# Performance work log

Measured on AMD Instinct MI355X. Metric: run time of the kernel, lower is better.

The kernel has to match this reference:

```python
import jax, jax.numpy as jnp
import numpy as np
from jax import lax

DIM = 128
NUM_HEADS = 8
GROUP_SPLIT = (4, 4)
DIM_HEAD = DIM // NUM_HEADS  # 16
SCALOR = DIM_HEAD ** (-0.5)
KSIZE = 5
WS = 4
C_HI = GROUP_SPLIT[0] * DIM_HEAD  # 64
C_LO = GROUP_SPLIT[1] * DIM_HEAD  # 64


def conv1x1(x, w, b):
    # x: [b,c,h,w], w: [o,c], b: [o]
    return jnp.einsum('oc,bchw->bohw', w, x) + b[None, :, None, None]


def dwconv(x, w, b):
    # depthwise conv, w: [C,1,k,k]
    C = x.shape[1]
    pad = KSIZE // 2
    y = lax.conv_general_dilated(x, w, window_strides=(1, 1),
                                 padding=((pad, pad), (pad, pad)),
                                 dimension_numbers=('NCHW', 'OIHW', 'NCHW'),
                                 feature_group_count=C)
    return y + b[None, :, None, None]


def avgpool(x, ws):
    b, c, h, w = x.shape
    return x.reshape(b, c, h // ws, ws, w // ws, ws).mean(axis=(3, 5))


def setup_inputs() -> dict:
    key = jax.random.key(0)
    ks = jax.random.split(key, 16)
    s = 0.02
    inp = {
        'x': jax.random.normal(ks[0], (8, DIM, 96, 96), dtype=jnp.float32),
        'qkv_w': jax.random.normal(ks[1], (3 * C_HI, DIM), dtype=jnp.float32) * s,
        'qkv_b': jnp.zeros((3 * C_HI,), jnp.float32),
        'dw_w': jax.random.normal(ks[2], (3 * C_HI, 1, KSIZE, KSIZE), dtype=jnp.float32) * s,
        'dw_b': jnp.zeros((3 * C_HI,), jnp.float32),
        'am_w1': jax.random.normal(ks[3], (C_HI, C_HI), dtype=jnp.float32) * s,
        'am_b1': jnp.zeros((C_HI,), jnp.float32),
        'am_w2': jax.random.normal(ks[4], (C_HI, C_HI), dtype=jnp.float32) * s,
        'am_b2': jnp.zeros((C_HI,), jnp.float32),
        'gq_w': jax.random.normal(ks[5], (C_LO, DIM), dtype=jnp.float32) * s,
        'gq_b': jnp.zeros((C_LO,), jnp.float32),
        'gkv_w': jax.random.normal(ks[6], (2 * C_LO, DIM), dtype=jnp.float32) * s,
        'gkv_b': jnp.zeros((2 * C_LO,), jnp.float32),
        'proj_w': jax.random.normal(ks[7], (DIM, DIM), dtype=jnp.float32) * s,
        'proj_b': jnp.zeros((DIM,), jnp.float32),
    }
    return inp


def reference(x, qkv_w, qkv_b, dw_w, dw_b, am_w1, am_b1, am_w2, am_b2,
              gq_w, gq_b, gkv_w, gkv_b, proj_w, proj_b):
    b, c, h, w = x.shape
    # ---- high-frequency branch ----
    qkv = dwconv(conv1x1(x, qkv_w, qkv_b), dw_w, dw_b)  # [b, 3*C_HI, h, w]
    qkv = qkv.reshape(b, 3, C_HI, h, w)
    q, k, v = qkv[:, 0], qkv[:, 1], qkv[:, 2]
    a = conv1x1(q * k, am_w1, am_b1)
    a = a * jax.nn.sigmoid(a)  # swish
    a = conv1x1(a, am_w2, am_b2) * SCALOR
    hi = jnp.tanh(a) * v  # [b, C_HI, h, w]
    # ---- low-frequency (windowed global) branch ----
    nq = h * w
    nk = nq // (WS * WS)
    q = conv1x1(x, gq_w, gq_b).reshape(b, GROUP_SPLIT[1], DIM_HEAD, nq)
    q = q.transpose(0, 1, 3, 2)  # [b, H, nq, dh]
    kv = conv1x1(avgpool(x, WS), gkv_w, gkv_b)  # [b, 2*C_LO, h/ws, w/ws]
    kv = kv.reshape(b, 2, GROUP_SPLIT[1], DIM_HEAD, nk)
    kk = kv[:, 0].transpose(0, 1, 3, 2)  # [b, H, nk, dh]
    vv = kv[:, 1].transpose(0, 1, 3, 2)
    attn = jax.nn.softmax(SCALOR * jnp.einsum('bhqd,bhkd->bhqk', q, kk), axis=-1)
    lo = jnp.einsum('bhqk,bhkd->bhqd', attn, vv)  # [b, H, nq, dh]
    lo = lo.transpose(0, 1, 3, 2).reshape(b, C_LO, h, w)
    # ---- merge + projection ----
    out = jnp.concatenate([hi, lo], axis=1)
    return conv1x1(out, proj_w, proj_b)
```

## Files before the change

### kernel.cpp

```cpp
#include <hip/hip_runtime.h>
#include <hip/hip_bf16.h>
#include <hip/hip_fp16.h>
#include <cstdint>

static constexpr int NB  = 8;
static constexpr int HH  = 96;
static constexpr int WW  = 96;
static constexpr int NP  = 9216;
static constexpr int NPK = 576;

using bf8 = __attribute__((ext_vector_type(8))) short;
using f4  = __attribute__((ext_vector_type(4))) float;

__device__ __forceinline__ unsigned pack_bf2(float a, float b) {
    __hip_bfloat162 h = __float22bfloat162_rn(make_float2(a, b));
    unsigned u; __builtin_memcpy(&u, &h, 4);
    return u;
}
__device__ __forceinline__ unsigned short f2bfu(float f) {
    __hip_bfloat16 h = __float2bfloat16(f);
    unsigned short u; __builtin_memcpy(&u, &h, 2);
    return u;
}
__device__ __forceinline__ float bf2f(unsigned short u) {
// ... 22 lines not shown
    const float* __restrict__ am_w2, const float* __restrict__ proj_w,
    unsigned* __restrict__ pw)
{
    const int idx = blockIdx.x * 256 + threadIdx.x;
    if (idx >= PW_TOTAL) return;
    const float* src; int j2; float sc = 1.0f;
    if (idx < PW_GQ)          { src = qkv_w;  j2 = (idx - PW_QKV) * 2; }
    else if (idx < PW_GKV)    { src = gq_w;   j2 = (idx - PW_GQ) * 2;  sc = 0.25f; }
    else if (idx < PW_AM1)    { src = gkv_w;  j2 = (idx - PW_GKV) * 2; }
    else if (idx < PW_AM2)    { src = am_w1;  j2 = (idx - PW_AM1) * 2; }
    else if (idx < PW_PROJ)   { src = am_w2;  j2 = (idx - PW_AM2) * 2; }
    else                      { src = proj_w; j2 = (idx - PW_PROJ) * 2; }
    pw[idx] = pack_bf2(src[j2] * sc, src[j2 + 1] * sc);
}

__global__ __launch_bounds__(256) void k_qkvgq(
    const float* __restrict__ x, const unsigned* __restrict__ pw,
    const float* __restrict__ qkv_b, const float* __restrict__ gq_b,
    unsigned short* __restrict__ qkv_out,
    unsigned short* __restrict__ gq_out)
{
    __shared__ __align__(16) unsigned xl[64 * 64];
    const int tid  = threadIdx.x;
    const int lane = tid & 63, wid = tid >> 6;
    const int quad = blockIdx.x, b = blockIdx.z;
    const int arow = lane & 15, agrp = lane >> 4;

    const float* xb = x + (long long)b * 128 * NP + quad * 64;

#pragma unroll
    for (int it = 0; it < 4; ++it) {
        const int task = tid + 256 * it;
        const int cp = task >> 4, pq = task & 15;
        float4 a = *(const float4*)&xb[(long long)(2 * cp) * NP + pq * 4];
        float4 c = *(const float4*)&xb[(long long)(2 * cp + 1) * NP + pq * 4];
        const int cps = cp ^ ((pq & 7) << 2);
        xl[(pq * 4 + 0) * 64 + cps] = pack_bf2(a.x, c.x);
        xl[(pq * 4 + 1) * 64 + cps] = pack_bf2(a.y, c.y);
        xl[(pq * 4 + 2) * 64 + cps] = pack_bf2(a.z, c.z);
        xl[(pq * 4 + 3) * 64 + cps] = pack_bf2(a.w, c.w);
// ... 37 lines not shown

        unsigned short* ob = isgq ? gq_out : qkv_out;
        const int ostride = isgq ? 64 : 192;
#pragma unroll
        for (int r = 0; r < 4; ++r) {
            const int o = och + agrp * 4 + r;
            const float bs = bsrc[o] * bsc;
            const float v0 = acc[0][r] + bs, v1 = acc[1][r] + bs;
            const float v2 = acc[2][r] + bs, v3 = acc[3][r] + bs;
            *(uint2*)&ob[((long long)b * ostride + o) * NP + quad * 64 + arow * 4] =
                make_uint2(pack_bf2(v0, v1), pack_bf2(v2, v3));
        }
    }
}

template<int C, int OT, int INBF, int OUTBF>
__global__ __launch_bounds__(256) void k_mfma_conv(
    const void* __restrict__ in0v, const unsigned* __restrict__ pw,
    const float* __restrict__ bias, void* __restrict__ outv,
    int np, long long ibs, int storeO)
{
    constexpr int KT = C / 32;
    const int tid  = threadIdx.x;
    const int lane = tid & 63, wid = tid >> 6;
    const int b    = blockIdx.z;
    const int obq  = blockIdx.y * (OT * 16);
    const int arow = lane & 15, agrp = lane >> 4;
    const int nquad = np >> 6;

    bf8 afr[OT][KT];
#pragma unroll
    for (int ot = 0; ot < OT; ++ot)
#pragma unroll
        for (int kt = 0; kt < KT; ++kt) {
            uint4 t = *(const uint4*)&pw[(obq + ot * 16 + arow) * (C / 2) + kt * 16 + agrp * 4];
            afr[ot][kt] = __builtin_bit_cast(bf8, t);
        }

    const float*          x0f = (const float*)in0v          + (long long)b * (INBF ? 0 : ibs);
    const unsigned short* x0h = (const unsigned short*)in0v + (long long)b * (INBF ? ibs : 0);

    const int quad = blockIdx.x * 4 + wid;
    if (quad >= nquad) return;
    const int p0 = quad * 64 + arow * 4;

    f4 acc[4][OT];
#pragma unroll
    for (int i = 0; i < 4; ++i)
#pragma unroll
        for (int ot = 0; ot < OT; ++ot) acc[i][ot] = (f4){0.f, 0.f, 0.f, 0.f};

#pragma unroll
    for (int kt = 0; kt < KT; ++kt) {
        const long long cbase = kt * 32 + agrp * 8;
        int uu[4][4];
#pragma unroll
        for (int jj = 0; jj < 4; ++jj) {
            if (INBF == 0) {
                float4 a0 = *(const float4*)&x0f[(cbase + 2 * jj) * np + p0];
                float4 a1 = *(const float4*)&x0f[(cbase + 2 * jj + 1) * np + p0];
                uu[0][jj] = (int)pack_bf2(a0.x, a1.x);
                uu[1][jj] = (int)pack_bf2(a0.y, a1.y);
                uu[2][jj] = (int)pack_bf2(a0.z, a1.z);
                uu[3][jj] = (int)pack_bf2(a0.w, a1.w);
            } else {
                ushort4 a0 = *(const ushort4*)&x0h[(cbase + 2 * jj) * np + p0];
                ushort4 a1 = *(const ushort4*)&x0h[(cbase + 2 * jj + 1) * np + p0];
                uu[0][jj] = (int)((unsigned)a0.x | ((unsigned)a1.x << 16));
                uu[1][jj] = (int)((unsigned)a0.y | ((unsigned)a1.y << 16));
                uu[2][jj] = (int)((unsigned)a0.z | ((unsigned)a1.z << 16));
                uu[3][jj] = (int)((unsigned)a0.w | ((unsigned)a1.w << 16));
            }
        }
#pragma unroll
        for (int i = 0; i < 4; ++i) {
            int4 ti = {uu[i][0], uu[i][1], uu[i][2], uu[i][3]};
            bf8 bfr = __builtin_bit_cast(bf8, ti);
#pragma unroll
            for (int ot = 0; ot < OT; ++ot)
                acc[i][ot] = __builtin_amdgcn_mfma_f32_16x16x32_bf16(afr[ot][kt], bfr, acc[i][ot], 0, 0, 0);
        }
    }

#pragma unroll
    for (int ot = 0; ot < OT; ++ot) {
#pragma unroll
        for (int r = 0; r < 4; ++r) {
            const int o = obq + ot * 16 + agrp * 4 + r;
            const float bs = bias[o];
            float4 v;
            v.x = acc[0][ot][r] + bs;
            v.y = acc[1][ot][r] + bs;
            v.z = acc[2][ot][r] + bs;
            v.w = acc[3][ot][r] + bs;
            const long long idx = ((long long)b * storeO + o) * np + p0;
            if (OUTBF == 0) {
                *(float4*)&((float*)outv)[idx] = v;
            } else {
                *(uint2*)&((unsigned short*)outv)[idx] =
                    make_uint2(pack_bf2(v.x, v.y), pack_bf2(v.z, v.w));
            }
        }
    }
}

__global__ __launch_bounds__(256) void k_am_attn(
    const unsigned short* __restrict__ dw, const unsigned* __restrict__ pw,
    const float* __restrict__ b1v, const float* __restrict__ b2v,
    const unsigned short* __restrict__ q, const float* __restrict__ kv,
    unsigned short* __restrict__ hilo)
{
    __shared__ __align__(16) char smem[53760];
    const int bid = blockIdx.x;
    const int tid = threadIdx.x;
    const int lane = tid & 63, wid = tid >> 6;

    if (bid < 576) {
        uint2* abuf = (uint2*)smem;
        const int arow = lane & 15, agrp = lane >> 4;

        const int hqi = bid * 4 + wid;
        const int b   = hqi / 288;
        const int t288 = hqi % 288;
        const int quad = t288 >> 1, half = t288 & 1;
        const int pp = quad * 64 + arow * 4 + half * 2;

        bf8 afr1[4][2], afr2[4][2];
#pragma unroll
        for (int ot = 0; ot < 4; ++ot)
#pragma unroll
            for (int kt = 0; kt < 2; ++kt) {
                uint4 t1 = *(const uint4*)&pw[PW_AM1 + (ot * 16 + arow) * 32 + kt * 16 + agrp * 4];
                uint4 t2 = *(const uint4*)&pw[PW_AM2 + (ot * 16 + arow) * 32 + kt * 16 + agrp * 4];
                afr1[ot][kt] = __builtin_bit_cast(bf8, t1);
                afr2[ot][kt] = __builtin_bit_cast(bf8, t2);
            }

        const unsigned short* xq = dw + (long long)b * (192ll * NP);
        const unsigned short* xk = xq + 64ll * NP;
        const unsigned short* xv = xq + 128ll * NP;

        f4 acc1[2][4];
#pragma unroll
        for (int i = 0; i < 2; ++i)
#pragma unroll
            for (int ot = 0; ot < 4; ++ot) acc1[i][ot] = (f4){0.f, 0.f, 0.f, 0.f};

#pragma unroll
        for (int kt = 0; kt < 2; ++kt) {
            const long long cbase = kt * 32 + agrp * 8;
            int uu[2][4];
#pragma unroll
            for (int jj = 0; jj < 4; ++jj) {
                ushort2 a0 = *(const ushort2*)&xq[(cbase + 2 * jj) * NP + pp];
                ushort2 a1 = *(const ushort2*)&xq[(cbase + 2 * jj + 1) * NP + pp];
                ushort2 y0 = *(const ushort2*)&xk[(cbase + 2 * jj) * NP + pp];
                ushort2 y1 = *(const ushort2*)&xk[(cbase + 2 * jj + 1) * NP + pp];
                uu[0][jj] = (int)pack_bf2(bf2f(a0.x) * bf2f(y0.x), bf2f(a1.x) * bf2f(y1.x));
                uu[1][jj] = (int)pack_bf2(bf2f(a0.y) * bf2f(y0.y), bf2f(a1.y) * bf2f(y1.y));
            }
#pragma unroll
            for (int i = 0; i < 2; ++i) {
                int4 ti = {uu[i][0], uu[i][1], uu[i][2], uu[i][3]};
                bf8 bfr = __builtin_bit_cast(bf8, ti);
#pragma unroll
                for (int ot = 0; ot < 4; ++ot)
                    acc1[i][ot] = __builtin_amdgcn_mfma_f32_16x16x32_bf16(afr1[ot][kt], bfr, acc1[i][ot], 0, 0, 0);
            }
        }

#pragma unroll
        for (int i = 0; i < 2; ++i)
#pragma unroll
            for (int ot = 0; ot < 4; ++ot) {
                const int ch0 = ot * 16 + agrp * 4;
                float v0 = acc1[i][ot][0] + b1v[ch0 + 0];
                float v1 = acc1[i][ot][1] + b1v[ch0 + 1];
                float v2 = acc1[i][ot][2] + b1v[ch0 + 2];
                float v3 = acc1[i][ot][3] + b1v[ch0 + 3];
                v0 = v0 / (1.f + __expf(-v0));
                v1 = v1 / (1.f + __expf(-v1));
                v2 = v2 / (1.f + __expf(-v2));
                v3 = v3 / (1.f + __expf(-v3));
                const int c2 = ot * 4 + agrp;
                abuf[wid * 512 + (arow * 2 + i) * 16 + (c2 ^ arow)] =
                    make_uint2(pack_bf2(v0, v1), pack_bf2(v2, v3));
            }

        f4 acc2[2][4];
#pragma unroll
        for (int i = 0; i < 2; ++i)
#pragma unroll
            for (int ot = 0; ot < 4; ++ot) acc2[i][ot] = (f4){0.f, 0.f, 0.f, 0.f};

#pragma unroll
        for (int kt = 0; kt < 2; ++kt) {
            const int bc2 = kt * 8 + agrp * 2;
#pragma unroll
            for (int i = 0; i < 2; ++i) {
                const uint2 rA = abuf[wid * 512 + (arow * 2 + i) * 16 + (bc2 ^ arow)];
                const uint2 rB = abuf[wid * 512 + (arow * 2 + i) * 16 + ((bc2 + 1) ^ arow)];
                int4 ti = make_int4((int)rA.x, (int)rA.y, (int)rB.x, (int)rB.y);
                bf8 bfr = __builtin_bit_cast(bf8, ti);
#pragma unroll
                for (int ot = 0; ot < 4; ++ot)
                    acc2[i][ot] = __builtin_amdgcn_mfma_f32_16x16x32_bf16(afr2[ot][kt], bfr, acc2[i][ot], 0, 0, 0);
            }
        }

#pragma unroll
        for (int ot = 0; ot < 4; ++ot) {
#pragma unroll
            for (int r = 0; r < 4; ++r) {
                const int o = ot * 16 + agrp * 4 + r;
                const float bs = b2v[o];
                ushort2 vv2 = *(const ushort2*)&xv[(long long)o * NP + pp];
                float h0 = tanhf((acc2[0][ot][r] + bs) * 0.25f) * bf2f(vv2.x);
                float h1 = tanhf((acc2[1][ot][r] + bs) * 0.25f) * bf2f(vv2.y);
                *(unsigned*)&hilo[((long long)b * 128 + o) * NP + pp] = pack_bf2(h0, h1);
            }
        }
        return;
    }

    int4*  klds4 = (int4*)smem;
    int4*  zlds4 = (int4*)(smem + 18432);
    int4*  vlds4 = (int4*)(smem + 18944);
    uint2* elds2 = (uint2*)(smem + 37376);

    const int flat = bid - 576;
    const int bx = flat % 72, bh = flat / 72;
    const int g = lane >> 4, qi = lane & 15;
    const int b = bh >> 2, h = bh & 3;

    const float* kbase = kv + ((long long)b * 128 + h * 16) * NPK;
    const float* vbase = kv + ((long long)b * 128 + 64 + h * 16) * NPK;

    for (int i = tid; i < 1152; i += 256) {
        const int key = i >> 1, dg = i & 1;
        const float* kp = kbase + (long long)(dg * 8) * NPK + key;
        int4 t;
        t.x = (int)pack_bf2(kp[0],       kp[NPK]);
        t.y = (int)pack_bf2(kp[2 * NPK], kp[3 * NPK]);
        t.z = (int)pack_bf2(kp[4 * NPK], kp[5 * NPK]);
        t.w = (int)pack_bf2(kp[6 * NPK], kp[7 * NPK]);
        klds4[(key >> 4) * 32 + dg * 16 + (key & 15)] = t;
    }
    for (int i = tid; i < 1152; i += 256) {
        const int t = i >> 6, l = i & 63;
        const float* vp = vbase + (long long)(l & 15) * NPK + t * 32 + (l >> 4) * 8;
        float4 a = *(const float4*)vp;
        float4 c = *(const float4*)(vp + 4);
        int4 tt;
        tt.x = (int)pack_bf2(a.x, a.y);
        tt.y = (int)pack_bf2(a.z, a.w);
        tt.z = (int)pack_bf2(c.x, c.y);
        tt.w = (int)pack_bf2(c.z, c.w);
        vlds4[i] = tt;
    }
    if (tid < 32) zlds4[tid] = make_int4(0, 0, 0, 0);
    __syncthreads();

    const int q0 = (bx * 4 + wid) * 32;
    const unsigned short* qcol = q + ((long long)b * 64 + h * 16) * NP + q0 + qi;
    int4 qv[2] = { make_int4(0, 0, 0, 0), make_int4(0, 0, 0, 0) };
    if (g < 2) {
#pragma unroll
        for (int s = 0; s < 2; ++s) {
            const unsigned short* qp = qcol + s * 16 + (long long)(g * 8) * NP;
            qv[s].x = (int)((unsigned)qp[0]          | ((unsigned)qp[(long long)NP]     << 16));
            qv[s].y = (int)((unsigned)qp[2ll * NP]   | ((unsigned)qp[3ll * NP]          << 16));
            qv[s].z = (int)((unsigned)qp[4ll * NP]   | ((unsigned)qp[5ll * NP]          << 16));
            qv[s].w = (int)((unsigned)qp[6ll * NP]   | ((unsigned)qp[7ll * NP]          << 16));
        }
    }

    f4 accp[2] = { (f4){0.f, 0.f, 0.f, 0.f}, (f4){0.f, 0.f, 0.f, 0.f} };
    float den[2] = { 0.f, 0.f };

    auto QKEXP = [&](int k2, int buf) {
#pragma unroll
        for (int tp = 0; tp < 2; ++tp) {
            const int4 kf = (lane < 32) ? klds4[(k2 * 2 + tp) * 32 + lane]
                                        : zlds4[lane & 31];
            const bf8 ka = __builtin_bit_cast(bf8, kf);
#pragma unroll
            for (int s = 0; s < 2; ++s) {
                f4 sa = __builtin_amdgcn_mfma_f32_16x16x32_bf16(
                    ka, __builtin_bit_cast(bf8, qv[s]), (f4){0.f, 0.f, 0.f, 0.f}, 0, 0, 0);
                const float e0 = __expf(sa[0]), e1 = __expf(sa[1]);
                const float e2 = __expf(sa[2]), e3 = __expf(sa[3]);
                den[s] += (e0 + e1) + (e2 + e3);
                elds2[buf * 1024 + wid * 256 + s * 128 + tp * 64 + g * 16 + qi] =
                    make_uint2(pack_bf2(e0, e1), pack_bf2(e2, e3));
            }
        }
    };
    auto PV = [&](int k2, int buf) {
        const bf8 va = __builtin_bit_cast(bf8, vlds4[k2 * 64 + lane]);
#pragma unroll
        for (int s = 0; s < 2; ++s) {
            const int base = buf * 1024 + wid * 256 + s * 128 + (g >> 1) * 64 + (g & 1) * 32 + qi;
            const uint2 r0 = elds2[base];
            const uint2 r1 = elds2[base + 16];
            int4 ti = make_int4((int)r0.x, (int)r0.y, (int)r1.x, (int)r1.y);
            accp[s] = __builtin_amdgcn_mfma_f32_16x16x32_bf16(
                va, __builtin_bit_cast(bf8, ti), accp[s], 0, 0, 0);
        }
    };

    QKEXP(0, 0);
    for (int k2 = 0; k2 < 17; ++k2) {
        QKEXP(k2 + 1, (k2 + 1) & 1);
        PV(k2, k2 & 1);
    }
    PV(17, 1);

#pragma unroll
    for (int s = 0; s < 2; ++s) {
        float d0 = den[s];
        d0 += __shfl_xor(d0, 16, 64);
        d0 += __shfl_xor(d0, 32, 64);
        const float inv = 1.0f / d0;
        unsigned short* op = hilo + ((long long)b * 128 + 64 + h * 16 + g * 4) * NP + q0 + s * 16 + qi;
#pragma unroll
        for (int r = 0; r < 4; ++r)
            op[(long long)r * NP] = f2bfu(accp[s][r] * inv);
    }
}

__global__ __launch_bounds__(256) void k_dwconv5_lds(
    const unsigned short* __restrict__ in, const float* __restrict__ w,
    const float* __restrict__ bias, unsigned short* __restrict__ out, int ch_total)
{
    __shared__ __align__(16) float img[36 * WW];
    const int tid = threadIdx.x;
    const int ch  = blockIdx.x;
    const int rt  = blockIdx.y;
    const int b   = blockIdx.z;
    const unsigned short* ip = in + ((long long)b * ch_total + ch) * NP;

    const int gr0 = rt * 32 - 2;
    for (int idx = tid; idx < 864; idx += 256) {
        const int rr = idx / 24, c4 = (idx - rr * 24) * 4;
        const int gr = gr0 + rr;
        float4 f;
        if (gr >= 0 && gr < HH) {
            const uint2 rv = *(const uint2*)&ip[gr * WW + c4];
            f.x = bflo(rv.x); f.y = bfhi(rv.x);
            f.z = bflo(rv.y); f.w = bfhi(rv.y);
        } else {
            f = make_float4(0.f, 0.f, 0.f, 0.f);
        }
        *(float4*)&img[rr * WW + c4] = f;
    }
    __syncthreads();

    const float* wp = w + ch * 25;
    float wr[25];
#pragma unroll
    for (int i = 0; i < 25; ++i) wr[i] = wp[i];
    const float bs = bias[ch];

    unsigned short* op = out + ((long long)b * ch_total + ch) * NP + rt * 32 * WW;

#pragma unroll
    for (int j = 0; j < 3; ++j) {
        const int q  = tid + 256 * j;
        const int yl = q / 24;
        const int x4 = (q - yl * 24) * 4;
        float o0 = bs, o1 = bs, o2 = bs, o3 = bs;
#pragma unroll
        for (int ky = 0; ky < 5; ++ky) {
            const float* row = &img[(yl + ky) * WW + x4];
            float4 mid = *(const float4*)row;
            float4 lf  = (x4 >= 4)      ? *(const float4*)(row - 4)
                                        : make_float4(0.f, 0.f, 0.f, 0.f);
            float4 rtv = (x4 + 4 < WW)  ? *(const float4*)(row + 4)
                                        : make_float4(0.f, 0.f, 0.f, 0.f);
// ... 4 lines not shown
                        w2 = wr[ky * 5 + 2], w3 = wr[ky * 5 + 3],
                        w4 = wr[ky * 5 + 4];
            o0 = fmaf(w0, f0, o0); o0 = fmaf(w1, f1, o0); o0 = fmaf(w2, f2, o0);
            o0 = fmaf(w3, f3, o0); o0 = fmaf(w4, f4v, o0);
            o1 = fmaf(w0, f1, o1); o1 = fmaf(w1, f2, o1); o1 = fmaf(w2, f3, o1);
            o1 = fmaf(w3, f4v, o1); o1 = fmaf(w4, f5, o1);
            o2 = fmaf(w0, f2, o2); o2 = fmaf(w1, f3, o2); o2 = fmaf(w2, f4v, o2);
            o2 = fmaf(w3, f5, o2); o2 = fmaf(w4, f6, o2);
            o3 = fmaf(w0, f3, o3); o3 = fmaf(w1, f4v, o3); o3 = fmaf(w2, f5, o3);
            o3 = fmaf(w3, f6, o3); o3 = fmaf(w4, f7, o3);
        }
        *(uint2*)&op[yl * WW + x4] = make_uint2(pack_bf2(o0, o1), pack_bf2(o2, o3));
    }
}

__global__ __launch_bounds__(256) void k_avgpool4(
    const float* __restrict__ in, float* __restrict__ out)
{
    int idx = blockIdx.x * 256 + threadIdx.x;
    int total = NB * 128 * NPK;
    if (idx >= total) return;
    int pw = idx % 24;
    int t  = idx / 24;
    int ph = t % 24;  t /= 24;
    int c  = t % 128;
    int b  = t / 128;
    const float* ip = in + ((long long)b * 128 + c) * NP + (ph * 4) * WW + pw * 4;
    float4 r0 = *(const float4*)(ip);
    float4 r1 = *(const float4*)(ip + WW);
    float4 r2 = *(const float4*)(ip + 2 * WW);
    float4 r3 = *(const float4*)(ip + 3 * WW);
    float s = ((r0.x + r0.y) + (r0.z + r0.w)) + ((r1.x + r1.y) + (r1.z + r1.w))
            + ((r2.x + r2.y) + (r2.z + r2.w)) + ((r3.x + r3.y) + (r3.z + r3.w));
    out[idx] = s * (1.0f / 16.0f);
}

extern "C" void kernel_launch(void* const* d_in, const int* in_sizes, int n_in,
                              void* d_out, int out_size, void* d_ws, size_t ws_size,
                              hipStream_t stream)
{
    const float* x      = (const float*)d_in[0];
    const float* qkv_w  = (const float*)d_in[1];
    const float* qkv_b  = (const float*)d_in[2];
    const float* dw_w   = (const float*)d_in[3];
    const float* dw_b   = (const float*)d_in[4];
    const float* am_w1  = (const float*)d_in[5];
    const float* am_b1  = (const float*)d_in[6];
    const float* am_w2  = (const float*)d_in[7];
    const float* am_b2  = (const float*)d_in[8];
// ... 4 lines not shown
    const float* proj_w = (const float*)d_in[13];
    const float* proj_b = (const float*)d_in[14];
    float* out = (float*)d_out;
    char* wsb = (char*)d_ws;

    unsigned short* t_qkv  = (unsigned short*)wsb;
    unsigned short* t_hilo = (unsigned short*)wsb;
    unsigned short* t_dw   = (unsigned short*)(wsb + 28311552);
    unsigned short* t_gq   = (unsigned short*)(wsb + 56623104);
    float*          t_pool = (float*)(wsb + 66060288);
    float*          t_gkv  = (float*)(wsb + 68419584);
    unsigned*       t_pw   = (unsigned*)(wsb + 70778880);

    k_packw<<<dim3((PW_TOTAL + 255) / 256), 256, 0, stream>>>(
        qkv_w, gq_w, gkv_w, am_w1, am_w2, proj_w, t_pw);
    k_qkvgq<<<dim3(144, 1, NB), 256, 0, stream>>>(
        x, t_pw, qkv_b, gq_b, t_qkv, t_gq);
    k_dwconv5_lds<<<dim3(192, 3, NB), 256, 0, stream>>>(t_qkv, dw_w, dw_b, t_dw, 192);
    k_avgpool4<<<dim3((NB*128*NPK + 255)/256), 256, 0, stream>>>(x, t_pool);
    k_mfma_conv<128,4,0,0><<<dim3(3,2,NB), 256, 0, stream>>>(
        t_pool, t_pw + PW_GKV, gkv_b, t_gkv, NPK, (long long)128 * NPK, 128);
    k_am_attn<<<dim3(2880), 256, 0, stream>>>(
        t_dw, t_pw, am_b1, am_b2, t_gq, t_gkv, t_hilo);
    k_mfma_conv<128,4,1,0><<<dim3(36,2,NB), 256, 0, stream>>>(
        t_hilo, t_pw + PW_PROJ, proj_b, out, NP, (long long)128 * NP, 128);
}
```

Before: 144.2 us.

## Merge avgpool into qkv/gq kernel and gkv conv into dwconv launch

Folds the avgpool work into the first 1x1-conv kernel as extra blocks and folds the gkv 1x1 conv into the depthwise-conv kernel as extra blocks, going from seven launches to five. Independent work now shares launches, so small kernels can overlap and launch gaps shrink. The projection conv also switches from 4 to 2 output tiles per block with twice as many blocks in y. The risk is load imbalance and shared-memory or register pressure from the heterogeneous blocks in each merged kernel.

```diff
diff --git a/kernel.cpp b/kernel.cpp
--- a/kernel.cpp
+++ b/kernel.cpp
@@ -60,16 +60,38 @@
     pw[idx] = pack_bf2(src[j2] * sc, src[j2 + 1] * sc);
 }
 
-__global__ __launch_bounds__(256) void k_qkvgq(
+__global__ __launch_bounds__(256) void k_pool_qkvgq(
     const float* __restrict__ x, const unsigned* __restrict__ pw,
     const float* __restrict__ qkv_b, const float* __restrict__ gq_b,
     unsigned short* __restrict__ qkv_out,
-    unsigned short* __restrict__ gq_out)
+    unsigned short* __restrict__ gq_out,
+    float* __restrict__ pool_out)
 {
     __shared__ __align__(16) unsigned xl[64 * 64];
-    const int tid  = threadIdx.x;
+    const int bid = blockIdx.x;
+    const int tid = threadIdx.x;
+
+    if (bid < 2304) {
+        const int idx = bid * 256 + tid;
+        int pw4 = idx % 24;
+        int t  = idx / 24;
+        int ph = t % 24;  t /= 24;
+        int c  = t % 128;
+        int b  = t / 128;
+        const float* ip = x + ((long long)b * 128 + c) * NP + (ph * 4) * WW + pw4 * 4;
+        float4 r0 = *(const float4*)(ip);
+        float4 r1 = *(const float4*)(ip + WW);
+        float4 r2 = *(const float4*)(ip + 2 * WW);
+        float4 r3 = *(const float4*)(ip + 3 * WW);
+        float s = ((r0.x + r0.y) + (r0.z + r0.w)) + ((r1.x + r1.y) + (r1.z + r1.w))
+                + ((r2.x + r2.y) + (r2.z + r2.w)) + ((r3.x + r3.y) + (r3.z + r3.w));
+        pool_out[idx] = s * (1.0f / 16.0f);
+        return;
+    }
+
+    const int qq   = bid - 2304;
+    const int quad = qq % 144, b = qq / 144;
     const int lane = tid & 63, wid = tid >> 6;
-    const int quad = blockIdx.x, b = blockIdx.z;
     const int arow = lane & 15, agrp = lane >> 4;
 
     const float* xb = x + (long long)b * 128 * NP + quad * 64;
@@ -137,197 +159,62 @@
     }
 }
 
-template<int C, int OT, int INBF, int OUTBF>
-__global__ __launch_bounds__(256) void k_mfma_conv(
-    const void* __restrict__ in0v, const unsigned* __restrict__ pw,
-    const float* __restrict__ bias, void* __restrict__ outv,
-    int np, long long ibs, int storeO)
+__global__ __launch_bounds__(256) void k_gkv_dw(
+    const float* __restrict__ pool_in, const unsigned* __restrict__ pw,
+    const float* __restrict__ gkv_b, float* __restrict__ gkv_out,
+    const unsigned short* __restrict__ qkv_in, const float* __restrict__ dw_w,
+    const float* __restrict__ dw_b, unsigned short* __restrict__ dw_out)
 {
-    constexpr int KT = C / 32;
-    const int tid  = threadIdx.x;
+    __shared__ __align__(16) float img[36 * WW];
+    const int bid = blockIdx.x;
+    const int tid = threadIdx.x;
     const int lane = tid & 63, wid = tid >> 6;
-    const int b    = blockIdx.z;
-    const int obq  = blockIdx.y * (OT * 16);
-    const int arow = lane & 15, agrp = lane >> 4;
-    const int nquad = np >> 6;
-
-    bf8 afr[OT][KT];
-#pragma unroll
-    for (int ot = 0; ot < OT; ++ot)
-#pragma unroll
-        for (int kt = 0; kt < KT; ++kt) {
-            uint4 t = *(const uint4*)&pw[(obq + ot * 16 + arow) * (C / 2) + kt * 16 + agrp * 4];
-            afr[ot][kt] = __builtin_bit_cast(bf8, t);
-        }
-
-    const float*          x0f = (const float*)in0v          + (long long)b * (INBF ? 0 : ibs);
-    const unsigned short* x0h = (const unsigned short*)in0v + (long long)b * (INBF ? ibs : 0);
-
-    const int quad = blockIdx.x * 4 + wid;
-    if (quad >= nquad) return;
-    const int p0 = quad * 64 + arow * 4;
-
-    f4 acc[4][OT];
-#pragma unroll
-    for (int i = 0; i < 4; ++i)
-#pragma unroll
-        for (int ot = 0; ot < OT; ++ot) acc[i][ot] = (f4){0.f, 0.f, 0.f, 0.f};
-
-#pragma unroll
-    for (int kt = 0; kt < KT; ++kt) {
-        const long long cbase = kt * 32 + agrp * 8;
-        int uu[4][4];
-#pragma unroll
-        for (int jj = 0; jj < 4; ++jj) {
-            if (INBF == 0) {
-                float4 a0 = *(const float4*)&x0f[(cbase + 2 * jj) * np + p0];
-                float4 a1 = *(const float4*)&x0f[(cbase + 2 * jj + 1) * np + p0];
+
+    if (bid < 48) {
+        const int bx = bid % 3, by = (bid / 3) % 2, bz = bid / 6;
+        const int arow = lane & 15, agrp = lane >> 4;
+        const int obq = by * 64;
+        const int quad = bx * 4 + wid;
+        if (quad >= 9) return;
+        const int p0 = quad * 64 + arow * 4;
+
+        bf8 afr[4][4];
+#pragma unroll
+        for (int ot = 0; ot < 4; ++ot)
+#pragma unroll
+            for (int kt = 0; kt < 4; ++kt) {
+                uint4 t = *(const uint4*)&pw[PW_GKV + (obq + ot * 16 + arow) * 64 + kt * 16 + agrp * 4];
+                afr[ot][kt] = __builtin_bit_cast(bf8, t);
+            }
+
+        const float* x0f = pool_in + (long long)bz * 128 * NPK;
+
+        f4 acc[4][4];
+#pragma unroll
+        for (int i = 0; i < 4; ++i)
+#pragma unroll
+            for (int ot = 0; ot < 4; ++ot) acc[i][ot] = (f4){0.f, 0.f, 0.f, 0.f};
+
+#pragma unroll
+        for (int kt = 0; kt < 4; ++kt) {
+            const long long cbase = kt * 32 + agrp * 8;
+            int uu[4][4];
+#pragma unroll
+            for (int jj = 0; jj < 4; ++jj) {
+                float4 a0 = *(const float4*)&x0f[(cbase + 2 * jj) * NPK + p0];
+                float4 a1 = *(const float4*)&x0f[(cbase + 2 * jj + 1) * NPK + p0];
                 uu[0][jj] = (int)pack_bf2(a0.x, a1.x);
                 uu[1][jj] = (int)pack_bf2(a0.y, a1.y);
                 uu[2][jj] = (int)pack_bf2(a0.z, a1.z);
                 uu[3][jj] = (int)pack_bf2(a0.w, a1.w);
-            } else {
-                ushort4 a0 = *(const ushort4*)&x0h[(cbase + 2 * jj) * np + p0];
-                ushort4 a1 = *(const ushort4*)&x0h[(cbase + 2 * jj + 1) * np + p0];
-                uu[0][jj] = (int)((unsigned)a0.x | ((unsigned)a1.x << 16));
-                uu[1][jj] = (int)((unsigned)a0.y | ((unsigned)a1.y << 16));
-                uu[2][jj] = (int)((unsigned)a0.z | ((unsigned)a1.z << 16));
-                uu[3][jj] = (int)((unsigned)a0.w | ((unsigned)a1.w << 16));
-            }
-        }
-#pragma unroll
-        for (int i = 0; i < 4; ++i) {
-            int4 ti = {uu[i][0], uu[i][1], uu[i][2], uu[i][3]};
-            bf8 bfr = __builtin_bit_cast(bf8, ti);
-#pragma unroll
-            for (int ot = 0; ot < OT; ++ot)
-                acc[i][ot] = __builtin_amdgcn_mfma_f32_16x16x32_bf16(afr[ot][kt], bfr, acc[i][ot], 0, 0, 0);
-        }
-    }
-
-#pragma unroll
-    for (int ot = 0; ot < OT; ++ot) {
-#pragma unroll
-        for (int r = 0; r < 4; ++r) {
-            const int o = obq + ot * 16 + agrp * 4 + r;
-            const float bs = bias[o];
-            float4 v;
-            v.x = acc[0][ot][r] + bs;
-            v.y = acc[1][ot][r] + bs;
-            v.z = acc[2][ot][r] + bs;
-            v.w = acc[3][ot][r] + bs;
-            const long long idx = ((long long)b * storeO + o) * np + p0;
-            if (OUTBF == 0) {
-                *(float4*)&((float*)outv)[idx] = v;
-            } else {
-                *(uint2*)&((unsigned short*)outv)[idx] =
-                    make_uint2(pack_bf2(v.x, v.y), pack_bf2(v.z, v.w));
-            }
-        }
-    }
-}
-
-__global__ __launch_bounds__(256) void k_am_attn(
-    const unsigned short* __restrict__ dw, const unsigned* __restrict__ pw,
-    const float* __restrict__ b1v, const float* __restrict__ b2v,
-    const unsigned short* __restrict__ q, const float* __restrict__ kv,
-    unsigned short* __restrict__ hilo)
-{
-    __shared__ __align__(16) char smem[53760];
-    const int bid = blockIdx.x;
-    const int tid = threadIdx.x;
-    const int lane = tid & 63, wid = tid >> 6;
-
-    if (bid < 576) {
-        uint2* abuf = (uint2*)smem;
-        const int arow = lane & 15, agrp = lane >> 4;
-
-        const int hqi = bid * 4 + wid;
-        const int b   = hqi / 288;
-        const int t288 = hqi % 288;
-        const int quad = t288 >> 1, half = t288 & 1;
-        const int pp = quad * 64 + arow * 4 + half * 2;
-
-        bf8 afr1[4][2], afr2[4][2];
-#pragma unroll
-        for (int ot = 0; ot < 4; ++ot)
-#pragma unroll
-            for (int kt = 0; kt < 2; ++kt) {
-                uint4 t1 = *(const uint4*)&pw[PW_AM1 + (ot * 16 + arow) * 32 + kt * 16 + agrp * 4];
-                uint4 t2 = *(const uint4*)&pw[PW_AM2 + (ot * 16 + arow) * 32 + kt * 16 + agrp * 4];
-                afr1[ot][kt] = __builtin_bit_cast(bf8, t1);
-                afr2[ot][kt] = __builtin_bit_cast(bf8, t2);
-            }
-
-        const unsigned short* xq = dw + (long long)b * (192ll * NP);
-        const unsigned short* xk = xq + 64ll * NP;
-        const unsigned short* xv = xq + 128ll * NP;
-
-        f4 acc1[2][4];
-#pragma unroll
-        for (int i = 0; i < 2; ++i)
-#pragma unroll
-            for (int ot = 0; ot < 4; ++ot) acc1[i][ot] = (f4){0.f, 0.f, 0.f, 0.f};
-
-#pragma unroll
-        for (int kt = 0; kt < 2; ++kt) {
-            const long long cbase = kt * 32 + agrp * 8;
-            int uu[2][4];
-#pragma unroll
-            for (int jj = 0; jj < 4; ++jj) {
-                ushort2 a0 = *(const ushort2*)&xq[(cbase + 2 * jj) * NP + pp];
-                ushort2 a1 = *(const ushort2*)&xq[(cbase + 2 * jj + 1) * NP + pp];
-                ushort2 y0 = *(const ushort2*)&xk[(cbase + 2 * jj) * NP + pp];
-                ushort2 y1 = *(const ushort2*)&xk[(cbase + 2 * jj + 1) * NP + pp];
-                uu[0][jj] = (int)pack_bf2(bf2f(a0.x) * bf2f(y0.x), bf2f(a1.x) * bf2f(y1.x));
-                uu[1][jj] = (int)pack_bf2(bf2f(a0.y) * bf2f(y0.y), bf2f(a1.y) * bf2f(y1.y));
-            }
-#pragma unroll
-            for (int i = 0; i < 2; ++i) {
+            }
+#pragma unroll
+            for (int i = 0; i < 4; ++i) {
                 int4 ti = {uu[i][0], uu[i][1], uu[i][2], uu[i][3]};
                 bf8 bfr = __builtin_bit_cast(bf8, ti);
 #pragma unroll
                 for (int ot = 0; ot < 4; ++ot)
-                    acc1[i][ot] = __builtin_amdgcn_mfma_f32_16x16x32_bf16(afr1[ot][kt], bfr, acc1[i][ot], 0, 0, 0);
-            }
-        }
-
-#pragma unroll
-        for (int i = 0; i < 2; ++i)
-#pragma unroll
-            for (int ot = 0; ot < 4; ++ot) {
-                const int ch0 = ot * 16 + agrp * 4;
-                float v0 = acc1[i][ot][0] + b1v[ch0 + 0];
-                float v1 = acc1[i][ot][1] + b1v[ch0 + 1];
-                float v2 = acc1[i][ot][2] + b1v[ch0 + 2];
-                float v3 = acc1[i][ot][3] + b1v[ch0 + 3];
-                v0 = v0 / (1.f + __expf(-v0));
-                v1 = v1 / (1.f + __expf(-v1));
-                v2 = v2 / (1.f + __expf(-v2));
-                v3 = v3 / (1.f + __expf(-v3));
-                const int c2 = ot * 4 + agrp;
-                abuf[wid * 512 + (arow * 2 + i) * 16 + (c2 ^ arow)] =
-                    make_uint2(pack_bf2(v0, v1), pack_bf2(v2, v3));
-            }
-
-        f4 acc2[2][4];
-#pragma unroll
-        for (int i = 0; i < 2; ++i)
-#pragma unroll
-            for (int ot = 0; ot < 4; ++ot) acc2[i][ot] = (f4){0.f, 0.f, 0.f, 0.f};
-
-#pragma unroll
-        for (int kt = 0; kt < 2; ++kt) {
-            const int bc2 = kt * 8 + agrp * 2;
-#pragma unroll
-            for (int i = 0; i < 2; ++i) {
-                const uint2 rA = abuf[wid * 512 + (arow * 2 + i) * 16 + (bc2 ^ arow)];
-                const uint2 rB = abuf[wid * 512 + (arow * 2 + i) * 16 + ((bc2 + 1) ^ arow)];
-                int4 ti = make_int4((int)rA.x, (int)rA.y, (int)rB.x, (int)rB.y);
-                bf8 bfr = __builtin_bit_cast(bf8, ti);
-#pragma unroll
-                for (int ot = 0; ot < 4; ++ot)
-                    acc2[i][ot] = __builtin_amdgcn_mfma_f32_16x16x32_bf16(afr2[ot][kt], bfr, acc2[i][ot], 0, 0, 0);
+                    acc[i][ot] = __builtin_amdgcn_mfma_f32_16x16x32_bf16(afr[ot][kt], bfr, acc[i][ot], 0, 0, 0);
             }
         }
 
@@ -335,133 +222,24 @@
         for (int ot = 0; ot < 4; ++ot) {
 #pragma unroll
             for (int r = 0; r < 4; ++r) {
-                const int o = ot * 16 + agrp * 4 + r;
-                const float bs = b2v[o];
-                ushort2 vv2 = *(const ushort2*)&xv[(long long)o * NP + pp];
-                float h0 = tanhf((acc2[0][ot][r] + bs) * 0.25f) * bf2f(vv2.x);
-                float h1 = tanhf((acc2[1][ot][r] + bs) * 0.25f) * bf2f(vv2.y);
-                *(unsigned*)&hilo[((long long)b * 128 + o) * NP + pp] = pack_bf2(h0, h1);
+                const int o = obq + ot * 16 + agrp * 4 + r;
+                const float bs = gkv_b[o];
+                float4 v;
+                v.x = acc[0][ot][r] + bs;
+                v.y = acc[1][ot][r] + bs;
+                v.z = acc[2][ot][r] + bs;
+                v.w = acc[3][ot][r] + bs;
+                *(float4*)&gkv_out[((long long)bz * 128 + o) * NPK + p0] = v;
             }
         }
         return;
     }
 
-    int4*  klds4 = (int4*)smem;
-    int4*  zlds4 = (int4*)(smem + 18432);
-    int4*  vlds4 = (int4*)(smem + 18944);
-    uint2* elds2 = (uint2*)(smem + 37376);
-
-    const int flat = bid - 576;
-    const int bx = flat % 72, bh = flat / 72;
-    const int g = lane >> 4, qi = lane & 15;
-    const int b = bh >> 2, h = bh & 3;
-
-    const float* kbase = kv + ((long long)b * 128 + h * 16) * NPK;
-    const float* vbase = kv + ((long long)b * 128 + 64 + h * 16) * NPK;
-
-    for (int i = tid; i < 1152; i += 256) {
-        const int key = i >> 1, dg = i & 1;
-        const float* kp = kbase + (long long)(dg * 8) * NPK + key;
-        int4 t;
-        t.x = (int)pack_bf2(kp[0],       kp[NPK]);
-        t.y = (int)pack_bf2(kp[2 * NPK], kp[3 * NPK]);
-        t.z = (int)pack_bf2(kp[4 * NPK], kp[5 * NPK]);
-        t.w = (int)pack_bf2(kp[6 * NPK], kp[7 * NPK]);
-        klds4[(key >> 4) * 32 + dg * 16 + (key & 15)] = t;
-    }
-    for (int i = tid; i < 1152; i += 256) {
-        const int t = i >> 6, l = i & 63;
-        const float* vp = vbase + (long long)(l & 15) * NPK + t * 32 + (l >> 4) * 8;
-        float4 a = *(const float4*)vp;
-        float4 c = *(const float4*)(vp + 4);
-        int4 tt;
-        tt.x = (int)pack_bf2(a.x, a.y);
-        tt.y = (int)pack_bf2(a.z, a.w);
-        tt.z = (int)pack_bf2(c.x, c.y);
-        tt.w = (int)pack_bf2(c.z, c.w);
-        vlds4[i] = tt;
-    }
-    if (tid < 32) zlds4[tid] = make_int4(0, 0, 0, 0);
-    __syncthreads();
-
-    const int q0 = (bx * 4 + wid) * 32;
-    const unsigned short* qcol = q + ((long long)b * 64 + h * 16) * NP + q0 + qi;
-    int4 qv[2] = { make_int4(0, 0, 0, 0), make_int4(0, 0, 0, 0) };
-    if (g < 2) {
-#pragma unroll
-        for (int s = 0; s < 2; ++s) {
-            const unsigned short* qp = qcol + s * 16 + (long long)(g * 8) * NP;
-            qv[s].x = (int)((unsigned)qp[0]          | ((unsigned)qp[(long long)NP]     << 16));
-            qv[s].y = (int)((unsigned)qp[2ll * NP]   | ((unsigned)qp[3ll * NP]          << 16));
-            qv[s].z = (int)((unsigned)qp[4ll * NP]   | ((unsigned)qp[5ll * NP]          << 16));
-            qv[s].w = (int)((unsigned)qp[6ll * NP]   | ((unsigned)qp[7ll * NP]          << 16));
-        }
-    }
-
-    f4 accp[2] = { (f4){0.f, 0.f, 0.f, 0.f}, (f4){0.f, 0.f, 0.f, 0.f} };
-    float den[2] = { 0.f, 0.f };
-
-    auto QKEXP = [&](int k2, int buf) {
-#pragma unroll
-        for (int tp = 0; tp < 2; ++tp) {
-            const int4 kf = (lane < 32) ? klds4[(k2 * 2 + tp) * 32 + lane]
-                                        : zlds4[lane & 31];
-            const bf8 ka = __builtin_bit_cast(bf8, kf);
-#pragma unroll
-            for (int s = 0; s < 2; ++s) {
-                f4 sa = __builtin_amdgcn_mfma_f32_16x16x32_bf16(
-                    ka, __builtin_bit_cast(bf8, qv[s]), (f4){0.f, 0.f, 0.f, 0.f}, 0, 0, 0);
-                const float e0 = __expf(sa[0]), e1 = __expf(sa[1]);
-                const float e2 = __expf(sa[2]), e3 = __expf(sa[3]);
-                den[s] += (e0 + e1) + (e2 + e3);
-                elds2[buf * 1024 + wid * 256 + s * 128 + tp * 64 + g * 16 + qi] =
-                    make_uint2(pack_bf2(e0, e1), pack_bf2(e2, e3));
-            }
-        }
-    };
-    auto PV = [&](int k2, int buf) {
-        const bf8 va = __builtin_bit_cast(bf8, vlds4[k2 * 64 + lane]);
-#pragma unroll
-        for (int s = 0; s < 2; ++s) {
-            const int base = buf * 1024 + wid * 256 + s * 128 + (g >> 1) * 64 + (g & 1) * 32 + qi;
-            const uint2 r0 = elds2[base];
-            const uint2 r1 = elds2[base + 16];
-            int4 ti = make_int4((int)r0.x, (int)r0.y, (int)r1.x, (int)r1.y);
-            accp[s] = __builtin_amdgcn_mfma_f32_16x16x32_bf16(
-                va, __builtin_bit_cast(bf8, ti), accp[s], 0, 0, 0);
-        }
-    };
-
-    QKEXP(0, 0);
-    for (int k2 = 0; k2 < 17; ++k2) {
-        QKEXP(k2 + 1, (k2 + 1) & 1);
-        PV(k2, k2 & 1);
-    }
-    PV(17, 1);
-
-#pragma unroll
-    for (int s = 0; s < 2; ++s) {
-        float d0 = den[s];
-        d0 += __shfl_xor(d0, 16, 64);
-        d0 += __shfl_xor(d0, 32, 64);
-        const float inv = 1.0f / d0;
-        unsigned short* op = hilo + ((long long)b * 128 + 64 + h * 16 + g * 4) * NP + q0 + s * 16 + qi;
-#pragma unroll
-        for (int r = 0; r < 4; ++r)
-            op[(long long)r * NP] = f2bfu(accp[s][r] * inv);
-    }
-}
-
-__global__ __launch_bounds__(256) void k_dwconv5_lds(
-    const unsigned short* __restrict__ in, const float* __restrict__ w,
-    const float* __restrict__ bias, unsigned short* __restrict__ out, int ch_total)
-{
-    __shared__ __align__(16) float img[36 * WW];
-    const int tid = threadIdx.x;
-    const int ch  = blockIdx.x;
-    const int rt  = blockIdx.y;
-    const int b   = blockIdx.z;
-    const unsigned short* ip = in + ((long long)b * ch_total + ch) * NP;
+    const int dbid = bid - 48;
+    const int ch = dbid % 192;
+    const int rt = (dbid / 192) % 3;
+    const int b  = dbid / 576;
+    const unsigned short* ip = qkv_in + ((long long)b * 192 + ch) * NP;
 
     const int gr0 = rt * 32 - 2;
     for (int idx = tid; idx < 864; idx += 256) {
@@ -479,13 +257,13 @@
     }
     __syncthreads();
 
-    const float* wp = w + ch * 25;
+    const float* wp = dw_w + ch * 25;
     float wr[25];
 #pragma unroll
     for (int i = 0; i < 25; ++i) wr[i] = wp[i];
-    const float bs = bias[ch];
-
-    unsigned short* op = out + ((long long)b * ch_total + ch) * NP + rt * 32 * WW;
+    const float bs = dw_b[ch];
+
+    unsigned short* op = dw_out + ((long long)b * 192 + ch) * NP + rt * 32 * WW;
 
 #pragma unroll
     for (int j = 0; j < 3; ++j) {
@@ -520,25 +298,319 @@
     }
 }
 
-__global__ __launch_bounds__(256) void k_avgpool4(
-    const float* __restrict__ in, float* __restrict__ out)
+template<int C, int OT, int INBF, int OUTBF>
+__global__ __launch_bounds__(256) void k_mfma_conv(
+    const void* __restrict__ in0v, const unsigned* __restrict__ pw,
+    const float* __restrict__ bias, void* __restrict__ outv,
+    int np, long long ibs, int storeO)
 {
-    int idx = blockIdx.x * 256 + threadIdx.x;
-    int total = NB * 128 * NPK;
-    if (idx >= total) return;
-    int pw = idx % 24;
-    int t  = idx / 24;
-    int ph = t % 24;  t /= 24;
-    int c  = t % 128;
-    int b  = t / 128;
-    const float* ip = in + ((long long)b * 128 + c) * NP + (ph * 4) * WW + pw * 4;
-    float4 r0 = *(const float4*)(ip);
-    float4 r1 = *(const float4*)(ip + WW);
-    float4 r2 = *(const float4*)(ip + 2 * WW);
-    float4 r3 = *(const float4*)(ip + 3 * WW);
-    float s = ((r0.x + r0.y) + (r0.z + r0.w)) + ((r1.x + r1.y) + (r1.z + r1.w))
-            + ((r2.x + r2.y) + (r2.z + r2.w)) + ((r3.x + r3.y) + (r3.z + r3.w));
-    out[idx] = s * (1.0f / 16.0f);
+    constexpr int KT = C / 32;
+    const int tid  = threadIdx.x;
+    const int lane = tid & 63, wid = tid >> 6;
+    const int b    = blockIdx.z;
+    const int obq  = blockIdx.y * (OT * 16);
+    const int arow = lane & 15, agrp = lane >> 4;
+    const int nquad = np >> 6;
+
+    bf8 afr[OT][KT];
+#pragma unroll
+    for (int ot = 0; ot < OT; ++ot)
+#pragma unroll
+        for (int kt = 0; kt < KT; ++kt) {
+            uint4 t = *(const uint4*)&pw[(obq + ot * 16 + arow) * (C / 2) + kt * 16 + agrp * 4];
+            afr[ot][kt] = __builtin_bit_cast(bf8, t);
+        }
+
+    const float*          x0f = (const float*)in0v          + (long long)b * (INBF ? 0 : ibs);
+    const unsigned short* x0h = (const unsigned short*)in0v + (long long)b * (INBF ? ibs : 0);
+
+    const int quad = blockIdx.x * 4 + wid;
+    if (quad >= nquad) return;
+    const int p0 = quad * 64 + arow * 4;
+
+    f4 acc[4][OT];
+#pragma unroll
+    for (int i = 0; i < 4; ++i)
+#pragma unroll
+        for (int ot = 0; ot < OT; ++ot) acc[i][ot] = (f4){0.f, 0.f, 0.f, 0.f};
+
+#pragma unroll
+    for (int kt = 0; kt < KT; ++kt) {
+        const long long cbase = kt * 32 + agrp * 8;
+        int uu[4][4];
+#pragma unroll
+        for (int jj = 0; jj < 4; ++jj) {
+            if (INBF == 0) {
+                float4 a0 = *(const float4*)&x0f[(cbase + 2 * jj) * np + p0];
+                float4 a1 = *(const float4*)&x0f[(cbase + 2 * jj + 1) * np + p0];
+                uu[0][jj] = (int)pack_bf2(a0.x, a1.x);
+                uu[1][jj] = (int)pack_bf2(a0.y, a1.y);
+                uu[2][jj] = (int)pack_bf2(a0.z, a1.z);
+                uu[3][jj] = (int)pack_bf2(a0.w, a1.w);
+            } else {
+                ushort4 a0 = *(const ushort4*)&x0h[(cbase + 2 * jj) * np + p0];
+                ushort4 a1 = *(const ushort4*)&x0h[(cbase + 2 * jj + 1) * np + p0];
+                uu[0][jj] = (int)((unsigned)a0.x | ((unsigned)a1.x << 16));
+                uu[1][jj] = (int)((unsigned)a0.y | ((unsigned)a1.y << 16));
+                uu[2][jj] = (int)((unsigned)a0.z | ((unsigned)a1.z << 16));
+                uu[3][jj] = (int)((unsigned)a0.w | ((unsigned)a1.w << 16));
+            }
+        }
+#pragma unroll
+        for (int i = 0; i < 4; ++i) {
+            int4 ti = {uu[i][0], uu[i][1], uu[i][2], uu[i][3]};
+            bf8 bfr = __builtin_bit_cast(bf8, ti);
+#pragma unroll
+            for (int ot = 0; ot < OT; ++ot)
+                acc[i][ot] = __builtin_amdgcn_mfma_f32_16x16x32_bf16(afr[ot][kt], bfr, acc[i][ot], 0, 0, 0);
+        }
+    }
+
+#pragma unroll
+    for (int ot = 0; ot < OT; ++ot) {
+#pragma unroll
+        for (int r = 0; r < 4; ++r) {
+            const int o = obq + ot * 16 + agrp * 4 + r;
+            const float bs = bias[o];
+            float4 v;
+            v.x = acc[0][ot][r] + bs;
+            v.y = acc[1][ot][r] + bs;
+            v.z = acc[2][ot][r] + bs;
+            v.w = acc[3][ot][r] + bs;
+            const long long idx = ((long long)b * storeO + o) * np + p0;
+            if (OUTBF == 0) {
+                *(float4*)&((float*)outv)[idx] = v;
+            } else {
+                *(uint2*)&((unsigned short*)outv)[idx] =
+                    make_uint2(pack_bf2(v.x, v.y), pack_bf2(v.z, v.w));
+            }
+        }
+    }
+}
+
+__global__ __launch_bounds__(256) void k_am_attn(
+    const unsigned short* __restrict__ dw, const unsigned* __restrict__ pw,
+    const float* __restrict__ b1v, const float* __restrict__ b2v,
+    const unsigned short* __restrict__ q, const float* __restrict__ kv,
+    unsigned short* __restrict__ hilo)
+{
+    __shared__ __align__(16) char smem[53760];
+    const int bid = blockIdx.x;
+    const int tid = threadIdx.x;
+    const int lane = tid & 63, wid = tid >> 6;
+
+    if (bid < 576) {
+        uint2* abuf = (uint2*)smem;
+        const int arow = lane & 15, agrp = lane >> 4;
+
+        const int hqi = bid * 4 + wid;
+        const int b   = hqi / 288;
+        const int t288 = hqi % 288;
+        const int quad = t288 >> 1, half = t288 & 1;
+        const int pp = quad * 64 + arow * 4 + half * 2;
+
+        bf8 afr1[4][2], afr2[4][2];
+#pragma unroll
+        for (int ot = 0; ot < 4; ++ot)
+#pragma unroll
+            for (int kt = 0; kt < 2; ++kt) {
+                uint4 t1 = *(const uint4*)&pw[PW_AM1 + (ot * 16 + arow) * 32 + kt * 16 + agrp * 4];
+                uint4 t2 = *(const uint4*)&pw[PW_AM2 + (ot * 16 + arow) * 32 + kt * 16 + agrp * 4];
+                afr1[ot][kt] = __builtin_bit_cast(bf8, t1);
+                afr2[ot][kt] = __builtin_bit_cast(bf8, t2);
+            }
+
+        const unsigned short* xq = dw + (long long)b * (192ll * NP);
+        const unsigned short* xk = xq + 64ll * NP;
+        const unsigned short* xv = xq + 128ll * NP;
+
+        f4 acc1[2][4];
+#pragma unroll
+        for (int i = 0; i < 2; ++i)
+#pragma unroll
+            for (int ot = 0; ot < 4; ++ot) acc1[i][ot] = (f4){0.f, 0.f, 0.f, 0.f};
+
+#pragma unroll
+        for (int kt = 0; kt < 2; ++kt) {
+            const long long cbase = kt * 32 + agrp * 8;
+            int uu[2][4];
+#pragma unroll
+            for (int jj = 0; jj < 4; ++jj) {
+                ushort2 a0 = *(const ushort2*)&xq[(cbase + 2 * jj) * NP + pp];
+                ushort2 a1 = *(const ushort2*)&xq[(cbase + 2 * jj + 1) * NP + pp];
+                ushort2 y0 = *(const ushort2*)&xk[(cbase + 2 * jj) * NP + pp];
+                ushort2 y1 = *(const ushort2*)&xk[(cbase + 2 * jj + 1) * NP + pp];
+                uu[0][jj] = (int)pack_bf2(bf2f(a0.x) * bf2f(y0.x), bf2f(a1.x) * bf2f(y1.x));
+                uu[1][jj] = (int)pack_bf2(bf2f(a0.y) * bf2f(y0.y), bf2f(a1.y) * bf2f(y1.y));
+            }
+#pragma unroll
+            for (int i = 0; i < 2; ++i) {
+                int4 ti = {uu[i][0], uu[i][1], uu[i][2], uu[i][3]};
+                bf8 bfr = __builtin_bit_cast(bf8, ti);
+#pragma unroll
+                for (int ot = 0; ot < 4; ++ot)
+                    acc1[i][ot] = __builtin_amdgcn_mfma_f32_16x16x32_bf16(afr1[ot][kt], bfr, acc1[i][ot], 0, 0, 0);
+            }
+        }
+
+#pragma unroll
+        for (int i = 0; i < 2; ++i)
+#pragma unroll
+            for (int ot = 0; ot < 4; ++ot) {
+                const int ch0 = ot * 16 + agrp * 4;
+                float v0 = acc1[i][ot][0] + b1v[ch0 + 0];
+                float v1 = acc1[i][ot][1] + b1v[ch0 + 1];
+                float v2 = acc1[i][ot][2] + b1v[ch0 + 2];
+                float v3 = acc1[i][ot][3] + b1v[ch0 + 3];
+                v0 = v0 / (1.f + __expf(-v0));
+                v1 = v1 / (1.f + __expf(-v1));
+                v2 = v2 / (1.f + __expf(-v2));
+                v3 = v3 / (1.f + __expf(-v3));
+                const int c2 = ot * 4 + agrp;
+                abuf[wid * 512 + (arow * 2 + i) * 16 + (c2 ^ arow)] =
+                    make_uint2(pack_bf2(v0, v1), pack_bf2(v2, v3));
+            }
+
+        f4 acc2[2][4];
+#pragma unroll
+        for (int i = 0; i < 2; ++i)
+#pragma unroll
+            for (int ot = 0; ot < 4; ++ot) acc2[i][ot] = (f4){0.f, 0.f, 0.f, 0.f};
+
+#pragma unroll
+        for (int kt = 0; kt < 2; ++kt) {
+            const int bc2 = kt * 8 + agrp * 2;
+#pragma unroll
+            for (int i = 0; i < 2; ++i) {
+                const uint2 rA = abuf[wid * 512 + (arow * 2 + i) * 16 + (bc2 ^ arow)];
+                const uint2 rB = abuf[wid * 512 + (arow * 2 + i) * 16 + ((bc2 + 1) ^ arow)];
+                int4 ti = make_int4((int)rA.x, (int)rA.y, (int)rB.x, (int)rB.y);
+                bf8 bfr = __builtin_bit_cast(bf8, ti);
+#pragma unroll
+                for (int ot = 0; ot < 4; ++ot)
+                    acc2[i][ot] = __builtin_amdgcn_mfma_f32_16x16x32_bf16(afr2[ot][kt], bfr, acc2[i][ot], 0, 0, 0);
+            }
+        }
+
+#pragma unroll
+        for (int ot = 0; ot < 4; ++ot) {
+#pragma unroll
+            for (int r = 0; r < 4; ++r) {
+                const int o = ot * 16 + agrp * 4 + r;
+                const float bs = b2v[o];
+                ushort2 vv2 = *(const ushort2*)&xv[(long long)o * NP + pp];
+                float h0 = tanhf((acc2[0][ot][r] + bs) * 0.25f) * bf2f(vv2.x);
+                float h1 = tanhf((acc2[1][ot][r] + bs) * 0.25f) * bf2f(vv2.y);
+                *(unsigned*)&hilo[((long long)b * 128 + o) * NP + pp] = pack_bf2(h0, h1);
+            }
+        }
+        return;
+    }
+
+    int4*  klds4 = (int4*)smem;
+    int4*  zlds4 = (int4*)(smem + 18432);
+    int4*  vlds4 = (int4*)(smem + 18944);
+    uint2* elds2 = (uint2*)(smem + 37376);
+
+    const int flat = bid - 576;
+    const int bx = flat % 72, bh = flat / 72;
+    const int g = lane >> 4, qi = lane & 15;
+    const int b = bh >> 2, h = bh & 3;
+
+    const float* kbase = kv + ((long long)b * 128 + h * 16) * NPK;
+    const float* vbase = kv + ((long long)b * 128 + 64 + h * 16) * NPK;
+
+    for (int i = tid; i < 1152; i += 256) {
+        const int key = i >> 1, dg = i & 1;
+        const float* kp = kbase + (long long)(dg * 8) * NPK + key;
+        int4 t;
+        t.x = (int)pack_bf2(kp[0],       kp[NPK]);
+        t.y = (int)pack_bf2(kp[2 * NPK], kp[3 * NPK]);
+        t.z = (int)pack_bf2(kp[4 * NPK], kp[5 * NPK]);
+        t.w = (int)pack_bf2(kp[6 * NPK], kp[7 * NPK]);
+        klds4[(key >> 4) * 32 + dg * 16 + (key & 15)] = t;
+    }
+    for (int i = tid; i < 1152; i += 256) {
+        const int t = i >> 6, l = i & 63;
+        const float* vp = vbase + (long long)(l & 15) * NPK + t * 32 + (l >> 4) * 8;
+        float4 a = *(const float4*)vp;
+        float4 c = *(const float4*)(vp + 4);
+        int4 tt;
+        tt.x = (int)pack_bf2(a.x, a.y);
+        tt.y = (int)pack_bf2(a.z, a.w);
+        tt.z = (int)pack_bf2(c.x, c.y);
+        tt.w = (int)pack_bf2(c.z, c.w);
+        vlds4[i] = tt;
+    }
+    if (tid < 32) zlds4[tid] = make_int4(0, 0, 0, 0);
+    __syncthreads();
+
+    const int q0 = (bx * 4 + wid) * 32;
+    const unsigned short* qcol = q + ((long long)b * 64 + h * 16) * NP + q0 + qi;
+    int4 qv[2] = { make_int4(0, 0, 0, 0), make_int4(0, 0, 0, 0) };
+    if (g < 2) {
+#pragma unroll
+        for (int s = 0; s < 2; ++s) {
+            const unsigned short* qp = qcol + s * 16 + (long long)(g * 8) * NP;
+            qv[s].x = (int)((unsigned)qp[0]          | ((unsigned)qp[(long long)NP]     << 16));
+            qv[s].y = (int)((unsigned)qp[2ll * NP]   | ((unsigned)qp[3ll * NP]          << 16));
+            qv[s].z = (int)((unsigned)qp[4ll * NP]   | ((unsigned)qp[5ll * NP]          << 16));
+            qv[s].w = (int)((unsigned)qp[6ll * NP]   | ((unsigned)qp[7ll * NP]          << 16));
+        }
+    }
+
+    f4 accp[2] = { (f4){0.f, 0.f, 0.f, 0.f}, (f4){0.f, 0.f, 0.f, 0.f} };
+    float den[2] = { 0.f, 0.f };
+
+    auto QKEXP = [&](int k2, int buf) {
+#pragma unroll
+        for (int tp = 0; tp < 2; ++tp) {
+            const int4 kf = (lane < 32) ? klds4[(k2 * 2 + tp) * 32 + lane]
+                                        : zlds4[lane & 31];
+            const bf8 ka = __builtin_bit_cast(bf8, kf);
+#pragma unroll
+            for (int s = 0; s < 2; ++s) {
+                f4 sa = __builtin_amdgcn_mfma_f32_16x16x32_bf16(
+                    ka, __builtin_bit_cast(bf8, qv[s]), (f4){0.f, 0.f, 0.f, 0.f}, 0, 0, 0);
+                const float e0 = __expf(sa[0]), e1 = __expf(sa[1]);
+                const float e2 = __expf(sa[2]), e3 = __expf(sa[3]);
+                den[s] += (e0 + e1) + (e2 + e3);
+                elds2[buf * 1024 + wid * 256 + s * 128 + tp * 64 + g * 16 + qi] =
+                    make_uint2(pack_bf2(e0, e1), pack_bf2(e2, e3));
+            }
+        }
+    };
+    auto PV = [&](int k2, int buf) {
+        const bf8 va = __builtin_bit_cast(bf8, vlds4[k2 * 64 + lane]);
+#pragma unroll
+        for (int s = 0; s < 2; ++s) {
+            const int base = buf * 1024 + wid * 256 + s * 128 + (g >> 1) * 64 + (g & 1) * 32 + qi;
+            const uint2 r0 = elds2[base];
+            const uint2 r1 = elds2[base + 16];
+            int4 ti = make_int4((int)r0.x, (int)r0.y, (int)r1.x, (int)r1.y);
+            accp[s] = __builtin_amdgcn_mfma_f32_16x16x32_bf16(
+                va, __builtin_bit_cast(bf8, ti), accp[s], 0, 0, 0);
+        }
+    };
+
+    QKEXP(0, 0);
+    for (int k2 = 0; k2 < 17; ++k2) {
+        QKEXP(k2 + 1, (k2 + 1) & 1);
+        PV(k2, k2 & 1);
+    }
+    PV(17, 1);
+
+#pragma unroll
+    for (int s = 0; s < 2; ++s) {
+        float d0 = den[s];
+        d0 += __shfl_xor(d0, 16, 64);
+        d0 += __shfl_xor(d0, 32, 64);
+        const float inv = 1.0f / d0;
+        unsigned short* op = hilo + ((long long)b * 128 + 64 + h * 16 + g * 4) * NP + q0 + s * 16 + qi;
+#pragma unroll
+        for (int r = 0; r < 4; ++r)
+            op[(long long)r * NP] = f2bfu(accp[s][r] * inv);
+    }
 }
 
 extern "C" void kernel_launch(void* const* d_in, const int* in_sizes, int n_in,
@@ -573,14 +645,12 @@
 
     k_packw<<<dim3((PW_TOTAL + 255) / 256), 256, 0, stream>>>(
         qkv_w, gq_w, gkv_w, am_w1, am_w2, proj_w, t_pw);
-    k_qkvgq<<<dim3(144, 1, NB), 256, 0, stream>>>(
-        x, t_pw, qkv_b, gq_b, t_qkv, t_gq);
-    k_dwconv5_lds<<<dim3(192, 3, NB), 256, 0, stream>>>(t_qkv, dw_w, dw_b, t_dw, 192);
-    k_avgpool4<<<dim3((NB*128*NPK + 255)/256), 256, 0, stream>>>(x, t_pool);
-    k_mfma_conv<128,4,0,0><<<dim3(3,2,NB), 256, 0, stream>>>(
-        t_pool, t_pw + PW_GKV, gkv_b, t_gkv, NPK, (long long)128 * NPK, 128);
+    k_pool_qkvgq<<<dim3(3456), 256, 0, stream>>>(
+        x, t_pw, qkv_b, gq_b, t_qkv, t_gq, t_pool);
+    k_gkv_dw<<<dim3(4656), 256, 0, stream>>>(
+        t_pool, t_pw, gkv_b, t_gkv, t_qkv, dw_w, dw_b, t_dw);
     k_am_attn<<<dim3(2880), 256, 0, stream>>>(
         t_dw, t_pw, am_b1, am_b2, t_gq, t_gkv, t_hilo);
-    k_mfma_conv<128,4,1,0><<<dim3(36,2,NB), 256, 0, stream>>>(
+    k_mfma_conv<128,2,1,0><<<dim3(36,4,NB), 256, 0, stream>>>(
         t_hilo, t_pw + PW_PROJ, proj_b, out, NP, (long long)128 * NP, 128);
 }
```

Result: slower. 154.3 us (+7.0%).
